# Performance work log

Hardware: AMD Instinct MI355X
Metric: run time of the kernel (lower is better)

The kernel has to match this reference:

```python
import jax, jax.numpy as jnp
import numpy as np

ALPHA = 0.25
GAMMA = 2.0
B, A, C, M = 8, 120000, 80, 32


def setup_inputs() -> dict:
    key = jax.random.key(0)
    k1, k2, k3, k4, k5, k6 = jax.random.split(key, 6)
    classifications = jax.random.uniform(k1, (B, A, C), jnp.float32)
    regressions = jax.random.normal(k2, (B, A, 4), jnp.float32)
    # anchors: valid x1<x2, y1<y2 boxes in a 1024x1024 image
    cx = jax.random.uniform(k3, (A,), jnp.float32, 0.0, 1024.0)
    cy = jax.random.uniform(k4, (A,), jnp.float32, 0.0, 1024.0)
    w = jax.random.uniform(jax.random.fold_in(k3, 1), (A,), jnp.float32, 16.0, 256.0)
    h = jax.random.uniform(jax.random.fold_in(k4, 1), (A,), jnp.float32, 16.0, 256.0)
    anchors = jnp.stack([cx - 0.5 * w, cy - 0.5 * h, cx + 0.5 * w, cy + 0.5 * h], axis=1)[None]
    # annotations: [x1,y1,x2,y2,label], all valid (label in [0, C))
    gcx = jax.random.uniform(k5, (B, M), jnp.float32, 64.0, 960.0)
    gcy = jax.random.uniform(jax.random.fold_in(k5, 1), (B, M), jnp.float32, 64.0, 960.0)
    gw = jax.random.uniform(jax.random.fold_in(k5, 2), (B, M), jnp.float32, 16.0, 256.0)
    gh = jax.random.uniform(jax.random.fold_in(k5, 3), (B, M), jnp.float32, 16.0, 256.0)
    labels = jax.random.randint(k6, (B, M), 0, C).astype(jnp.float32)
    annotations = jnp.stack(
        [gcx - 0.5 * gw, gcy - 0.5 * gh, gcx + 0.5 * gw, gcy + 0.5 * gh, labels], axis=2)
    return dict(classifications=classifications, regressions=regressions,
                anchors=anchors, annotations=annotations)


def _calc_iou(a, b):
    # a: [A,4] anchors, b: [M,4] gt boxes -> [A,M]
    area = (b[:, 2] - b[:, 0]) * (b[:, 3] - b[:, 1])
    iw = jnp.minimum(a[:, 2, None], b[None, :, 2]) - jnp.maximum(a[:, 0, None], b[None, :, 0])
    ih = jnp.minimum(a[:, 3, None], b[None, :, 3]) - jnp.maximum(a[:, 1, None], b[None, :, 1])
    inter = jnp.clip(iw, 0.0) * jnp.clip(ih, 0.0)
    ua = ((a[:, 2] - a[:, 0]) * (a[:, 3] - a[:, 1]))[:, None] + area[None, :] - inter
    return inter / jnp.clip(ua, 1e-8)


def _per_image(cls, reg, annots, anchor):
    valid = annots[:, 4] != -1.0  # padded gt boxes (label == -1) are ignored
    num_valid = valid.sum()
    cls = jnp.clip(cls, 1e-4, 1.0 - 1e-4)
    iou = jnp.where(valid[None, :], _calc_iou(anchor, annots[:, :4]), -1.0)  # [A,M]
    iou_max = iou.max(axis=1)
    iou_argmax = iou.argmax(axis=1)
    positive = iou_max >= 0.5
    num_pos = positive.sum()
    assigned = annots[iou_argmax]  # [A,5]
    nclass = cls.shape[1]
    # targets: -1 ignore; 0 where IoU<0.4 or positive; one-hot 1 at gt class for positives
    targets = jnp.full(cls.shape, -1.0, cls.dtype)
    targets = jnp.where((iou_max < 0.4)[:, None], 0.0, targets)
    onehot = jax.nn.one_hot(assigned[:, 4].astype(jnp.int32), nclass, dtype=cls.dtype)
    targets = jnp.where(positive[:, None], onehot, targets)
    alpha_factor = jnp.where(targets == 1.0, ALPHA, 1.0 - ALPHA)
    focal_w = alpha_factor * jnp.where(targets == 1.0, 1.0 - cls, cls) ** GAMMA
    bce = -(targets * jnp.log(cls) + (1.0 - targets) * jnp.log(1.0 - cls))
    cls_loss_mat = jnp.where(targets != -1.0, focal_w * bce, 0.0)
    npos_f = num_pos.astype(cls.dtype)
    cls_loss = cls_loss_mat.sum() / jnp.maximum(npos_f, 1.0)
    aw = anchor[:, 2] - anchor[:, 0]
    ah = anchor[:, 3] - anchor[:, 1]
    acx = anchor[:, 0] + 0.5 * aw
    acy = anchor[:, 1] + 0.5 * ah
    gw = assigned[:, 2] - assigned[:, 0]
    gh = assigned[:, 3] - assigned[:, 1]
    gcx = assigned[:, 0] + 0.5 * gw
    gcy = assigned[:, 1] + 0.5 * gh
    gw = jnp.maximum(gw, 1.0)
    gh = jnp.maximum(gh, 1.0)
    t = jnp.stack([(gcx - acx) / aw, (gcy - acy) / ah,
                   jnp.log(gw / aw), jnp.log(gh / ah)], axis=1)
    t = t / jnp.array([[0.1, 0.1, 0.2, 0.2]], t.dtype)
    diff = jnp.abs(t - reg)
    rl = jnp.where(diff <= 1.0 / 9.0, 0.5 * 9.0 * diff * diff, diff - 0.5 / 9.0)
    rl = jnp.where(positive[:, None], rl, 0.0)
    reg_loss = rl.sum() / jnp.maximum(npos_f * 4.0, 1.0)  # mean over [num_pos,4]
    reg_loss = jnp.where(num_pos > 0, reg_loss, 0.0)
    has = num_valid > 0
    return jnp.where(has, cls_loss, 0.0), jnp.where(has, reg_loss, 0.0)


def reference(classifications, regressions, anchors, annotations):
    anchor = anchors[0]
    cls_l, reg_l = jax.vmap(lambda c, r, a: _per_image(c, r, a, anchor))(
        classifications, regressions, annotations)
    return cls_l.mean(keepdims=True), reg_l.mean(keepdims=True)
```

## Files before the change

### kernel.cpp

```cpp
#include <hip/hip_runtime.h>

constexpr int B_IMG = 8;
constexpr int A_N   = 120000;
constexpr int C_N   = 80;
constexpr int M_N   = 32;

constexpr float ALPHA = 0.25f;

constexpr int BLK  = 256;
constexpr int APB  = 1024;
constexpr int NBLK = (A_N + APB - 1) / APB;
constexpr int F4PA = C_N / 4;
constexpr int U    = 4;
constexpr int F4_PER_IT = BLK * U;
constexpr int NIT  = (APB * F4PA) / F4_PER_IT;

typedef float f4v __attribute__((ext_vector_type(4)));

__device__ __forceinline__ float smooth_l1(float d) {
    d = fabsf(d);
    return (d <= (1.0f / 9.0f)) ? 4.5f * d * d : d - (0.5f / 9.0f);
}

__device__ __forceinline__ float loss_neg(float x) {
    float p = fminf(fmaxf(x, 1e-4f), 0.9999f);
    return (1.0f - ALPHA) * p * p * (-__logf(1.0f - p));
}

__device__ __forceinline__ float loss_neg4(f4v v) {
    return loss_neg(v[0]) + loss_neg(v[1]) + loss_neg(v[2]) + loss_neg(v[3]);
}

__device__ __forceinline__ float loss_pos(float x) {
    float p = fminf(fmaxf(x, 1e-4f), 0.9999f);
    float q = 1.0f - p;
    return ALPHA * q * q * (-__logf(p));
}

__device__ __forceinline__ signed char assign_one(
    const float4 anc, const float* __restrict__ ann,
    const float4* __restrict__ regs, int b, int a,
    float& regl, int& pcount)
{
    const float ax1 = anc.x, ay1 = anc.y, ax2 = anc.z, ay2 = anc.w;
    const float areaA = (ax2 - ax1) * (ay2 - ay1);

    float bi = -1.0f;
    float bu = 1.0f;
    int   bm = -1;
    #pragma unroll 2
    for (int m = 0; m < M_N; ++m) {
        const float gx1 = ann[m * 5 + 0];
        const float gy1 = ann[m * 5 + 1];
        const float gx2 = ann[m * 5 + 2];
        const float gy2 = ann[m * 5 + 3];
        const bool valid = (ann[m * 5 + 4] != -1.0f);
        float iw = fminf(ax2, gx2) - fmaxf(ax1, gx1);
        float ih = fminf(ay2, gy2) - fmaxf(ay1, gy1);
        iw = fmaxf(iw, 0.0f);
        ih = fmaxf(ih, 0.0f);
        const float inter = iw * ih;
        const float areaB = (gx2 - gx1) * (gy2 - gy1);
        const float ua = fmaxf(areaA + areaB - inter, 1e-8f);
        const bool better = valid && (inter * bu > bi * ua);
        if (better) { bi = inter; bu = ua; bm = m; }
    }

    const float iouMax = (bm >= 0) ? (bi / bu) : -1.0f;
    const bool positive = (iouMax >= 0.5f);

    if (positive) {
        pcount += 1;
        const float aw  = ax2 - ax1;
        const float ah  = ay2 - ay1;
        const float acx = ax1 + 0.5f * aw;
        const float acy = ay1 + 0.5f * ah;
        const float gx1 = ann[bm * 5 + 0];
        const float gy1 = ann[bm * 5 + 1];
        const float gx2 = ann[bm * 5 + 2];
        const float gy2 = ann[bm * 5 + 3];
        float gw = gx2 - gx1;
        float gh = gy2 - gy1;
        const float gcx = gx1 + 0.5f * gw;
        const float gcy = gy1 + 0.5f * gh;
        gw = fmaxf(gw, 1.0f);
        gh = fmaxf(gh, 1.0f);
        const float t0 = ((gcx - acx) / aw) * 10.0f;
        const float t1 = ((gcy - acy) / ah) * 10.0f;
        const float t2 = __logf(gw / aw) * 5.0f;
        const float t3 = __logf(gh / ah) * 5.0f;
        const float4 rg = regs[(size_t)b * A_N + a];
        regl += smooth_l1(t0 - rg.x) + smooth_l1(t1 - rg.y) +
                smooth_l1(t2 - rg.z) + smooth_l1(t3 - rg.w);
    }

    if (iouMax < 0.4f) return -1;
    if (positive)      return (signed char)(int)ann[bm * 5 + 4];
    return -2;
}

__global__ __launch_bounds__(BLK, 4) void fused_kernel(
    const float* __restrict__ cls,
    const float* __restrict__ regressions,
    const float* __restrict__ anchors,
    const float* __restrict__ annotations,
    float* __restrict__ clsPart,
    float* __restrict__ regPart,
    float* __restrict__ nposPart)
{
    const int b    = blockIdx.y;
    const int base = blockIdx.x * APB;
    const int nA   = min(APB, A_N - base);
    const float* __restrict__ ann = annotations + (size_t)b * M_N * 5;
    const float4* __restrict__ regs = (const float4*)regressions;

    __shared__ signed char scode[APB];
    __shared__ float       smask[APB];

    const int t    = threadIdx.x;
    const int wave = t >> 6;
    const int lane = t & 63;
    const bool full = (nA == APB);

    const float* __restrict__ rowbase = cls + (size_t)(b * A_N + base) * C_N;
    const f4v* __restrict__ src = (const f4v*)rowbase;
    const f4v* __restrict__ pw = src + wave * (64 * U) + lane;
    const int widx0 = wave * (64 * U) + lane;

    f4v vA[U], vB[U];
    if (full) {
        #pragma unroll
        for (int u = 0; u < U; ++u) vA[u] = pw[u * 64];
        #pragma unroll
        for (int u = 0; u < U; ++u) vB[u] = pw[F4_PER_IT + u * 64];
    }

    float regl = 0.0f;
    int   pcnt = 0;
    #pragma unroll 1
    for (int s = 0; s < APB; s += BLK) {
        const int li = s + t;
        const int a  = base + li;
        signed char c = -2;
        if (li < nA) {
            const float4 anc = ((const float4*)anchors)[a];
            c = assign_one(anc, ann, regs, b, a, regl, pcnt);
        }
        scode[li] = c;
        smask[li] = (c != -2) ? 1.0f : 0.0f;
    }
    __syncthreads();

    float csum = 0.0f;

    if (full) {
        #pragma unroll 1
        for (int it2 = 0; it2 < NIT / 2; ++it2) {
            const int it = it2 * 2;
            float pa = 0.0f;
            #pragma unroll
            for (int u = 0; u < U; ++u) {
                const unsigned idx = (unsigned)(it * F4_PER_IT + widx0 + u * 64);
                pa += smask[idx / 20u] * loss_neg4(vA[u]);
            }
            if (it + 2 < NIT) {
                #pragma unroll
                for (int u = 0; u < U; ++u)
                    vA[u] = pw[(it + 2) * F4_PER_IT + u * 64];
            }
            csum += pa;
            float pb = 0.0f;
            #pragma unroll
            for (int u = 0; u < U; ++u) {
                const unsigned idx = (unsigned)((it + 1) * F4_PER_IT + widx0 + u * 64);
                pb += smask[idx / 20u] * loss_neg4(vB[u]);
            }
            if (it + 3 < NIT) {
                #pragma unroll
                for (int u = 0; u < U; ++u)
                    vB[u] = pw[(it + 3) * F4_PER_IT + u * 64];
            }
            csum += pb;
        }
    } else {
        const int nF4 = nA * F4PA;
        for (int idx = t; idx < nF4; idx += BLK) {
            const f4v v = src[idx];
            csum += smask[(unsigned)idx / 20u] * loss_neg4(v);
        }
    }

    #pragma unroll 1
    for (int s = 0; s < APB; s += BLK) {
        const int li = s + t;
        const int code = scode[li];
        if (code >= 0) {
            const float x = rowbase[(size_t)li * C_N + code];
            csum += loss_pos(x) - loss_neg(x);
        }
    }

    float r = regl, p = (float)pcnt, c = csum;
    #pragma unroll
    for (int off = 32; off; off >>= 1) {
        r += __shfl_down(r, off);
        p += __shfl_down(p, off);
        c += __shfl_down(c, off);
    }
    __shared__ float wr[BLK / 64], wp[BLK / 64], wc[BLK / 64];
    if (lane == 0) { wr[wave] = r; wp[wave] = p; wc[wave] = c; }
    __syncthreads();
    if (t == 0) {
        float rr = 0.0f, pp = 0.0f, cc = 0.0f;
        #pragma unroll
        for (int w = 0; w < BLK / 64; ++w) { rr += wr[w]; pp += wp[w]; cc += wc[w]; }
        const int pidx = b * NBLK + blockIdx.x;
        clsPart[pidx]  = cc;
        regPart[pidx]  = rr;
        nposPart[pidx] = pp;
    }
}

__global__ __launch_bounds__(64 * B_IMG) void finalize_kernel(
    const float* __restrict__ annotations,
    const float* __restrict__ clsPart,
    const float* __restrict__ regPart,
    const float* __restrict__ nposPart,
    float* __restrict__ out)
{
    const int w    = threadIdx.x >> 6;
    const int lane = threadIdx.x & 63;

    float c = 0.0f, r = 0.0f, p = 0.0f;
    for (int i = lane; i < NBLK; i += 64) {
        const int idx = w * NBLK + i;
        c += clsPart[idx];
        r += regPart[idx];
        p += nposPart[idx];
    }
    #pragma unroll
    for (int off = 32; off; off >>= 1) {
        c += __shfl_down(c, off);
        r += __shfl_down(r, off);
        p += __shfl_down(p, off);
    }

    __shared__ float sc[B_IMG], sr[B_IMG];
    if (lane == 0) {
        bool has = false;
        for (int m = 0; m < M_N; ++m)
            has = has || (annotations[(size_t)w * M_N * 5 + m * 5 + 4] != -1.0f);
        const float cl = c / fmaxf(p, 1.0f);
        const float rl = (p > 0.0f) ? r / (p * 4.0f) : 0.0f;
        sc[w] = has ? cl : 0.0f;
        sr[w] = has ? rl : 0.0f;
    }
    __syncthreads();
    if (threadIdx.x == 0) {
        float ca = 0.0f, ra = 0.0f;
        #pragma unroll
        for (int i = 0; i < B_IMG; ++i) { ca += sc[i]; ra += sr[i]; }
        out[0] = ca * (1.0f / B_IMG);
        out[1] = ra * (1.0f / B_IMG);
    }
}

extern "C" void kernel_launch(void* const* d_in, const int* in_sizes, int n_in,
                              void* d_out, int out_size, void* d_ws, size_t ws_size,
                              hipStream_t stream) {
    const float* classifications = (const float*)d_in[0];
    const float* regressions     = (const float*)d_in[1];
    const float* anchors         = (const float*)d_in[2];
    const float* annotations     = (const float*)d_in[3];
    float* out = (float*)d_out;

    float* clsPart  = (float*)d_ws;
    float* regPart  = clsPart + (size_t)B_IMG * NBLK;
    float* nposPart = regPart + (size_t)B_IMG * NBLK;

    fused_kernel<<<dim3(NBLK, B_IMG), BLK, 0, stream>>>(
        classifications, regressions, anchors, annotations,
        clsPart, regPart, nposPart);

    finalize_kernel<<<1, 64 * B_IMG, 0, stream>>>(
        annotations, clsPart, regPart, nposPart, out);
}
```

Before: 85.75 us.

## Sum negative loss unmasked, then subtract ignored rows after anchor assignment

The streaming focal-loss pass now runs over all classification rows without first waiting for the per-anchor IoU assignment, so the shared-memory mask, its syncthreads, and the per-element mask lookups are removed. After the stream, each thread assigns its anchors and corrects the sum by subtracting the negative loss of ignored anchors (re-reading those rows) and applying the positive correction inline. The anchors-per-block count is halved, which doubles the block count. The cost is a re-read of the classification rows for ignored anchors and serialized assignment work at the end of each block.

```diff
diff --git a/kernel.cpp b/kernel.cpp
--- a/kernel.cpp
+++ b/kernel.cpp
@@ -8,12 +8,13 @@
 constexpr float ALPHA = 0.25f;
 
 constexpr int BLK  = 256;
-constexpr int APB  = 1024;
+constexpr int APB  = 512;
 constexpr int NBLK = (A_N + APB - 1) / APB;
 constexpr int F4PA = C_N / 4;
 constexpr int U    = 4;
 constexpr int F4_PER_IT = BLK * U;
 constexpr int NIT  = (APB * F4PA) / F4_PER_IT;
+constexpr int ApT  = APB / BLK;
 
 typedef float f4v __attribute__((ext_vector_type(4)));
 
@@ -35,68 +36,6 @@
     float p = fminf(fmaxf(x, 1e-4f), 0.9999f);
     float q = 1.0f - p;
     return ALPHA * q * q * (-__logf(p));
-}
-
-__device__ __forceinline__ signed char assign_one(
-    const float4 anc, const float* __restrict__ ann,
-    const float4* __restrict__ regs, int b, int a,
-    float& regl, int& pcount)
-{
-    const float ax1 = anc.x, ay1 = anc.y, ax2 = anc.z, ay2 = anc.w;
-    const float areaA = (ax2 - ax1) * (ay2 - ay1);
-
-    float bi = -1.0f;
-    float bu = 1.0f;
-    int   bm = -1;
-    #pragma unroll 2
-    for (int m = 0; m < M_N; ++m) {
-        const float gx1 = ann[m * 5 + 0];
-        const float gy1 = ann[m * 5 + 1];
-        const float gx2 = ann[m * 5 + 2];
-        const float gy2 = ann[m * 5 + 3];
-        const bool valid = (ann[m * 5 + 4] != -1.0f);
-        float iw = fminf(ax2, gx2) - fmaxf(ax1, gx1);
-        float ih = fminf(ay2, gy2) - fmaxf(ay1, gy1);
-        iw = fmaxf(iw, 0.0f);
-        ih = fmaxf(ih, 0.0f);
-        const float inter = iw * ih;
-        const float areaB = (gx2 - gx1) * (gy2 - gy1);
-        const float ua = fmaxf(areaA + areaB - inter, 1e-8f);
-        const bool better = valid && (inter * bu > bi * ua);
-        if (better) { bi = inter; bu = ua; bm = m; }
-    }
-
-    const float iouMax = (bm >= 0) ? (bi / bu) : -1.0f;
-    const bool positive = (iouMax >= 0.5f);
-
-    if (positive) {
-        pcount += 1;
-        const float aw  = ax2 - ax1;
-        const float ah  = ay2 - ay1;
-        const float acx = ax1 + 0.5f * aw;
-        const float acy = ay1 + 0.5f * ah;
-        const float gx1 = ann[bm * 5 + 0];
-        const float gy1 = ann[bm * 5 + 1];
-        const float gx2 = ann[bm * 5 + 2];
-        const float gy2 = ann[bm * 5 + 3];
-        float gw = gx2 - gx1;
-        float gh = gy2 - gy1;
-        const float gcx = gx1 + 0.5f * gw;
-        const float gcy = gy1 + 0.5f * gh;
-        gw = fmaxf(gw, 1.0f);
-        gh = fmaxf(gh, 1.0f);
-        const float t0 = ((gcx - acx) / aw) * 10.0f;
-        const float t1 = ((gcy - acy) / ah) * 10.0f;
-        const float t2 = __logf(gw / aw) * 5.0f;
-        const float t3 = __logf(gh / ah) * 5.0f;
-        const float4 rg = regs[(size_t)b * A_N + a];
-        regl += smooth_l1(t0 - rg.x) + smooth_l1(t1 - rg.y) +
-                smooth_l1(t2 - rg.z) + smooth_l1(t3 - rg.w);
-    }
-
-    if (iouMax < 0.4f) return -1;
-    if (positive)      return (signed char)(int)ann[bm * 5 + 4];
-    return -2;
 }
 
 __global__ __launch_bounds__(BLK, 4) void fused_kernel(
@@ -111,12 +50,6 @@
     const int b    = blockIdx.y;
     const int base = blockIdx.x * APB;
     const int nA   = min(APB, A_N - base);
-    const float* __restrict__ ann = annotations + (size_t)b * M_N * 5;
-    const float4* __restrict__ regs = (const float4*)regressions;
-
-    __shared__ signed char scode[APB];
-    __shared__ float       smask[APB];
-
     const int t    = threadIdx.x;
     const int wave = t >> 6;
     const int lane = t & 63;
@@ -125,44 +58,22 @@
     const float* __restrict__ rowbase = cls + (size_t)(b * A_N + base) * C_N;
     const f4v* __restrict__ src = (const f4v*)rowbase;
     const f4v* __restrict__ pw = src + wave * (64 * U) + lane;
-    const int widx0 = wave * (64 * U) + lane;
-
-    f4v vA[U], vB[U];
+
+    float csum = 0.0f;
+
     if (full) {
+        f4v vA[U], vB[U];
         #pragma unroll
         for (int u = 0; u < U; ++u) vA[u] = pw[u * 64];
         #pragma unroll
         for (int u = 0; u < U; ++u) vB[u] = pw[F4_PER_IT + u * 64];
-    }
-
-    float regl = 0.0f;
-    int   pcnt = 0;
-    #pragma unroll 1
-    for (int s = 0; s < APB; s += BLK) {
-        const int li = s + t;
-        const int a  = base + li;
-        signed char c = -2;
-        if (li < nA) {
-            const float4 anc = ((const float4*)anchors)[a];
-            c = assign_one(anc, ann, regs, b, a, regl, pcnt);
-        }
-        scode[li] = c;
-        smask[li] = (c != -2) ? 1.0f : 0.0f;
-    }
-    __syncthreads();
-
-    float csum = 0.0f;
-
-    if (full) {
+
         #pragma unroll 1
         for (int it2 = 0; it2 < NIT / 2; ++it2) {
             const int it = it2 * 2;
             float pa = 0.0f;
             #pragma unroll
-            for (int u = 0; u < U; ++u) {
-                const unsigned idx = (unsigned)(it * F4_PER_IT + widx0 + u * 64);
-                pa += smask[idx / 20u] * loss_neg4(vA[u]);
-            }
+            for (int u = 0; u < U; ++u) pa += loss_neg4(vA[u]);
             if (it + 2 < NIT) {
                 #pragma unroll
                 for (int u = 0; u < U; ++u)
@@ -171,10 +82,7 @@
             csum += pa;
             float pb = 0.0f;
             #pragma unroll
-            for (int u = 0; u < U; ++u) {
-                const unsigned idx = (unsigned)((it + 1) * F4_PER_IT + widx0 + u * 64);
-                pb += smask[idx / 20u] * loss_neg4(vB[u]);
-            }
+            for (int u = 0; u < U; ++u) pb += loss_neg4(vB[u]);
             if (it + 3 < NIT) {
                 #pragma unroll
                 for (int u = 0; u < U; ++u)
@@ -184,23 +92,83 @@
         }
     } else {
         const int nF4 = nA * F4PA;
-        for (int idx = t; idx < nF4; idx += BLK) {
-            const f4v v = src[idx];
-            csum += smask[(unsigned)idx / 20u] * loss_neg4(v);
+        for (int idx = t; idx < nF4; idx += BLK)
+            csum += loss_neg4(src[idx]);
+    }
+
+    const float* __restrict__ ann = annotations + (size_t)b * M_N * 5;
+    float regl = 0.0f, pos = 0.0f;
+
+    #pragma unroll 1
+    for (int sIt = 0; sIt < ApT; ++sIt) {
+        const int li = sIt * BLK + t;
+        const int a  = base + li;
+        if (li < nA) {
+            const float4 anc = ((const float4*)anchors)[a];
+            const float ax1 = anc.x, ay1 = anc.y, ax2 = anc.z, ay2 = anc.w;
+            const float areaA = (ax2 - ax1) * (ay2 - ay1);
+
+            float bi = -1.0f, bu = 1.0f;
+            int   bm = -1;
+            #pragma unroll 2
+            for (int m = 0; m < M_N; ++m) {
+                const float gx1 = ann[m * 5 + 0];
+                const float gy1 = ann[m * 5 + 1];
+                const float gx2 = ann[m * 5 + 2];
+                const float gy2 = ann[m * 5 + 3];
+                const bool valid = (ann[m * 5 + 4] != -1.0f);
+                float iw = fminf(ax2, gx2) - fmaxf(ax1, gx1);
+                float ih = fminf(ay2, gy2) - fmaxf(ay1, gy1);
+                iw = fmaxf(iw, 0.0f);
+                ih = fmaxf(ih, 0.0f);
+                const float inter = iw * ih;
+                const float areaB = (gx2 - gx1) * (gy2 - gy1);
+                const float ua = fmaxf(areaA + areaB - inter, 1e-8f);
+                const bool better = valid && (inter * bu > bi * ua);
+                if (better) { bi = inter; bu = ua; bm = m; }
+            }
+            const float iouMax = (bm >= 0) ? (bi / bu) : -1.0f;
+            const bool positive = (iouMax >= 0.5f);
+            const bool ignored  = (iouMax >= 0.4f) && !positive;
+
+            if (positive) {
+                pos += 1.0f;
+                const float aw  = ax2 - ax1;
+                const float ah  = ay2 - ay1;
+                const float acx = ax1 + 0.5f * aw;
+                const float acy = ay1 + 0.5f * ah;
+                const float gx1 = ann[bm * 5 + 0];
+                const float gy1 = ann[bm * 5 + 1];
+                const float gx2 = ann[bm * 5 + 2];
+                const float gy2 = ann[bm * 5 + 3];
+                float gw = gx2 - gx1;
+                float gh = gy2 - gy1;
+                const float gcx = gx1 + 0.5f * gw;
+                const float gcy = gy1 + 0.5f * gh;
+                gw = fmaxf(gw, 1.0f);
+                gh = fmaxf(gh, 1.0f);
+                const float t0 = ((gcx - acx) / aw) * 10.0f;
+                const float t1 = ((gcy - acy) / ah) * 10.0f;
+                const float t2 = __logf(gw / aw) * 5.0f;
+                const float t3 = __logf(gh / ah) * 5.0f;
+                const float4 rg = ((const float4*)regressions)[(size_t)b * A_N + a];
+                regl += smooth_l1(t0 - rg.x) + smooth_l1(t1 - rg.y) +
+                        smooth_l1(t2 - rg.z) + smooth_l1(t3 - rg.w);
+
+                const int code = (int)ann[bm * 5 + 4];
+                const float x = rowbase[(size_t)li * C_N + code];
+                csum += loss_pos(x) - loss_neg(x);
+            } else if (ignored) {
+                const f4v* __restrict__ row = (const f4v*)(rowbase + (size_t)li * C_N);
+                float rs = 0.0f;
+                #pragma unroll 4
+                for (int u = 0; u < C_N / 4; ++u) rs += loss_neg4(row[u]);
+                csum -= rs;
+            }
         }
     }
 
-    #pragma unroll 1
-    for (int s = 0; s < APB; s += BLK) {
-        const int li = s + t;
-        const int code = scode[li];
-        if (code >= 0) {
-            const float x = rowbase[(size_t)li * C_N + code];
-            csum += loss_pos(x) - loss_neg(x);
-        }
-    }
-
-    float r = regl, p = (float)pcnt, c = csum;
+    float r = regl, p = pos, c = csum;
     #pragma unroll
     for (int off = 32; off; off >>= 1) {
         r += __shfl_down(r, off);
```

Result: slower. 118.4 us (+38.1%).
